# Kernel tuning notes

Measured on AMD Instinct MI355X. Metric: run time of the kernel, lower is better.

The kernel has to match this reference:

```python
import jax, jax.numpy as jnp
import numpy as np

B, N_HEADS, F_TOK = 8, 12, 768
GRID_H, GRID_W = 32, 32
N_TOK = 1 + GRID_H * GRID_W  # 1025 (readout token + patches)
F_HEAD = F_TOK // N_HEADS    # 64
NUM_DIST = (2 * GRID_H - 1) * (2 * GRID_W - 1) + 3  # 3972


def _build_relpos_index(gh, gw):
    # BEiT-style relative position index with 3 extra slots for the readout token
    coords = np.stack(np.meshgrid(np.arange(gh), np.arange(gw), indexing='ij'))  # (2, gh, gw)
    flat = coords.reshape(2, -1)                                                 # (2, gh*gw)
    rel = flat[:, :, None] - flat[:, None, :]                                    # (2, P, P)
    rel = rel.transpose(1, 2, 0).astype(np.int64)                                # (P, P, 2)
    rel[:, :, 0] += gh - 1
    rel[:, :, 1] += gw - 1
    rel[:, :, 0] *= 2 * gw - 1
    rpi = rel.sum(-1)                                                            # (P, P)
    n = 1 + gh * gw
    nd = (2 * gh - 1) * (2 * gw - 1) + 3
    idx = np.zeros((n, n), dtype=np.int32)
    idx[1:, 1:] = rpi
    idx[0, :] = nd - 3  # readout -> all
    idx[:, 0] = nd - 2  # all -> readout
    idx[0, 0] = nd - 1  # readout -> readout
    return idx


def setup_inputs() -> dict:
    key = jax.random.key(0)
    ks = jax.random.split(key, 7)
    tokens = jax.random.normal(ks[0], (B, N_TOK, F_TOK), dtype=jnp.float32)
    qkv_w = jax.random.normal(ks[1], (3 * F_TOK, F_TOK), dtype=jnp.float32) * 0.02
    q_bias = jax.random.normal(ks[2], (1, N_HEADS, 1, F_HEAD), dtype=jnp.float32) * 0.02
    v_bias = jax.random.normal(ks[3], (1, N_HEADS, 1, F_HEAD), dtype=jnp.float32) * 0.02
    relpos_table = jax.random.normal(ks[4], (NUM_DIST, N_HEADS), dtype=jnp.float32) * 0.02
    proj_w = jax.random.normal(ks[5], (F_TOK, F_TOK), dtype=jnp.float32) * 0.02
    proj_b = jax.random.normal(ks[6], (F_TOK,), dtype=jnp.float32) * 0.02
    relpos_index = jnp.asarray(_build_relpos_index(GRID_H, GRID_W))  # (N, N) int32
    return {
        'tokens': tokens, 'qkv_w': qkv_w, 'q_bias': q_bias, 'v_bias': v_bias,
        'relpos_table': relpos_table, 'proj_w': proj_w, 'proj_b': proj_b,
        'relpos_index': relpos_index, 'patch_h': GRID_H, 'patch_w': GRID_W,
    }


def reference(tokens, qkv_w, q_bias, v_bias, relpos_table, proj_w, proj_b,
              relpos_index, patch_h, patch_w):
    b, n, f_tok = tokens.shape
    # qkv projection (no bias): (B, N, 3F) -> (3, B, H, N, f)
    qkv = tokens @ qkv_w.T
    qkv = qkv.reshape(b, n, 3, N_HEADS, F_HEAD).transpose(2, 0, 3, 1, 4)
    q, k, v = qkv[0], qkv[1], qkv[2]
    q = (q + q_bias) * (F_HEAD ** -0.5)
    v = v + v_bias
    # attention scores: (B, H, N, N)
    attn = jnp.einsum('bhnf,bhmf->bhnm', q, k)
    # relative position bias gather: (N, N, H) -> (H, N, N)
    bias = relpos_table[relpos_index].transpose(2, 0, 1)
    attn = attn + bias[None]
    w = jax.nn.softmax(attn, axis=-1)
    out = jnp.einsum('bhnm,bhmf->bhnf', w, v)
    out = out.transpose(0, 2, 1, 3).reshape(b, n, N_HEADS * F_HEAD)
    return out @ proj_w.T + proj_b
```

## Files before the change

### kernel.cpp

```cpp
#include <hip/hip_runtime.h>

#define B_ 8
#define NH 12
#define NTOK 1025
#define FT 768
#define MROWS (B_*NTOK)
#define QPAD 1025
#define CH2 34
#define NQT 36
#define NTT 34
#define NDIST 3972
#define LOG2E 1.44269504089f

typedef __bf16 bf16x8 __attribute__((ext_vector_type(8)));
typedef __bf16 bf16x2 __attribute__((ext_vector_type(2)));
typedef float floatx4 __attribute__((ext_vector_type(4)));
typedef float floatx16 __attribute__((ext_vector_type(16)));
typedef int intx4 __attribute__((ext_vector_type(4)));

__device__ __forceinline__ void async_ld16(const void* gp, void* lp) {
  __builtin_amdgcn_global_load_lds(
      (const __attribute__((address_space(1))) void*)gp,
      (__attribute__((address_space(3))) void*)lp, 16, 0, 0);
}

__global__ __launch_bounds__(256) void cvt_bf16(const float* __restrict__ src,
                                                __bf16* __restrict__ dst, int n4) {
  int i = blockIdx.x * 256 + threadIdx.x;
  if (i >= n4) return;
  float4 v = ((const float4*)src)[i];
  __bf16 o[4] = {(__bf16)v.x, (__bf16)v.y, (__bf16)v.z, (__bf16)v.w};
  *(uint2*)(dst + 4 * (size_t)i) = *(uint2*)o;
}

__global__ __launch_bounds__(256) void table_prep(const float* __restrict__ table,
                                                  __bf16* __restrict__ tableT) {
  int i = blockIdx.x * 256 + threadIdx.x;
  if (i >= NH * NDIST) return;
  int h = i / NDIST, d = i - h * NDIST;
  tableT[i] = (__bf16)(table[(size_t)d * NH + h] * LOG2E);
}

__global__ __launch_bounds__(256) void bias_gather_t(
    const int* __restrict__ idx, const __bf16* __restrict__ tableT,
    __bf16* __restrict__ Bb) {
  __shared__ int ids_l[32][33];
  const int qt = blockIdx.x, tt = blockIdx.y;
  const int t = threadIdx.x;
  {
    const int row = t >> 3, c4 = (t & 7) * 4;
    int qrow = qt * 32 + row; if (qrow > NTOK - 1) qrow = NTOK - 1;
    const int* src = idx + (size_t)qrow * NTOK;
#pragma unroll
    for (int j = 0; j < 4; ++j) {
      int token = tt * 32 + c4 + j; if (token > NTOK - 1) token = NTOK - 1;
      ids_l[row][c4 + j] = src[token];
    }
  }
  __syncthreads();
  const int lane = t & 63, w = t >> 6;
  const int l31 = lane & 31, hb = lane >> 5;
  int ids[16]; bool ok[16];
#pragma unroll
  for (int j = 0; j < 16; ++j) {
    const int col = (j & 3) + 8 * (j >> 2) + 4 * hb;
    ok[j] = tt * 32 + col < NTOK;
    ids[j] = ids_l[l31][col];
  }
#pragma unroll
  for (int g = 0; g < 3; ++g) {
    const int h = w + g * 4;
    const __bf16* tb = tableT + (size_t)h * NDIST;
    __bf16 v[16] __attribute__((aligned(16)));
#pragma unroll
    for (int j = 0; j < 16; ++j)
      v[j] = ok[j] ? tb[ids[j]] : (__bf16)(-1e30f);
    uint4* dst = (uint4*)(Bb + (((size_t)h * NQT + qt) * NTT + tt) * 1024 + lane * 16);
    dst[0] = ((uint4*)v)[0];
    dst[1] = ((uint4*)v)[1];
  }
}

__device__ __forceinline__ void gemm128_pipe(
    const __bf16* __restrict__ A, const __bf16* __restrict__ W,
    int am0, int n0, int amax, __bf16* At, __bf16* Bt, floatx4 acc[4][4]) {
  const int tid = threadIdx.x, wave = tid >> 6, lane = tid & 63;
  const int l = lane & 15, qd = lane >> 4;
  const int wr = wave >> 1, wc = wave & 1;
  const int srow = lane >> 2, sg = lane & 3;
  const int r0 = wave * 32 + srow, r1 = r0 + 16;
  int gm0 = am0 + r0; if (gm0 > amax) gm0 = amax;
  int gm1 = am0 + r1; if (gm1 > amax) gm1 = amax;
  const int sw0 = (sg ^ (r0 & 3)) * 8;
  const __bf16* gA0 = A + (size_t)gm0 * FT + sw0;
  const __bf16* gA1 = A + (size_t)gm1 * FT + sw0;
  const __bf16* gB0 = W + (size_t)(n0 + r0) * FT + sw0;
  const __bf16* gB1 = W + (size_t)(n0 + r1) * FT + sw0;
  const int woff = wave * 32 * 32;
  const int fsw = (qd ^ (l & 3)) * 8;

  auto issue = [&](int k, int buf) {
    __bf16* a = At + buf * 4096 + woff;
    __bf16* b = Bt + buf * 4096 + woff;
    async_ld16(gA0 + k * 32, a);
    async_ld16(gA1 + k * 32, a + 512);
    async_ld16(gB0 + k * 32, b);
    async_ld16(gB1 + k * 32, b + 512);
  };
  auto step = [&](int buf) {
    __builtin_amdgcn_s_barrier();
    const __bf16* ab = At + buf * 4096;
    const __bf16* bb = Bt + buf * 4096;
    bf16x8 aF[4], bF[4];
#pragma unroll
    for (int t = 0; t < 4; ++t)
      aF[t] = *(const bf16x8*)(ab + (wr * 64 + t * 16 + l) * 32 + fsw);
#pragma unroll
    for (int u = 0; u < 4; ++u)
      bF[u] = *(const bf16x8*)(bb + (wc * 64 + u * 16 + l) * 32 + fsw);
#pragma unroll
    for (int t = 0; t < 4; ++t)
#pragma unroll
      for (int u = 0; u < 4; ++u)
        acc[t][u] = __builtin_amdgcn_mfma_f32_16x16x32_bf16(aF[t], bF[u], acc[t][u], 0, 0, 0);
  };

  issue(0, 0);
  issue(1, 1);
  issue(2, 2);
  int b0 = 0, b3 = 3;
  for (int k = 0; k < 24; ++k) {
    if (k < 21) {
      issue(k + 3, b3);
      __builtin_amdgcn_s_waitcnt(0x0F7C);
    } else if (k == 21) {
      __builtin_amdgcn_s_waitcnt(0x0F78);
    } else if (k == 22) {
      __builtin_amdgcn_s_waitcnt(0x0F74);
    } else {
      __builtin_amdgcn_s_waitcnt(0x0F70);
    }
    step(b0);
    ++b0; if (b0 == 5) b0 = 0;
    ++b3; if (b3 == 5) b3 = 0;
  }
}

__global__ __launch_bounds__(256) void qkv_gemm128(
    const __bf16* __restrict__ tokens, const __bf16* __restrict__ qkvw,
    const float* __restrict__ qbias, const float* __restrict__ vbias,
    __bf16* __restrict__ Qb, __bf16* __restrict__ Kc, __bf16* __restrict__ Vc) {
  __shared__ __bf16 At[5 * 4096], Bt[5 * 4096];
  const int u0 = blockIdx.x;
  const int c = u0 & 7, q0 = u0 >> 3;
  const int mt = (q0 / 18) * 8 + c, ni = q0 % 18;
  const int b = mt / 9, ml = mt - b * 9;
  const int am0 = b * NTOK + ml * 128, amax = b * NTOK + 1024;
  const int n0 = ni * 128;
  const int tid = threadIdx.x, wave = tid >> 6, lane = tid & 63;
  const int l = lane & 15, qd = lane >> 4;
  const int wr = wave >> 1, wc = wave & 1;
  floatx4 acc[4][4];
#pragma unroll
  for (int t = 0; t < 4; ++t)
#pragma unroll
    for (int u = 0; u < 4; ++u) acc[t][u] = (floatx4){0.f, 0.f, 0.f, 0.f};
  gemm128_pipe(tokens, qkvw, am0, n0, amax, At, Bt, acc);

  const int which = ni / 6;
  const int nrem0 = (ni - which * 6) * 128;
  const bool full = (ml < 8);
  const int tokb = ml * 128 + wr * 64 + qd * 4;

  if (which == 0) {
#pragma unroll
    for (int u = 0; u < 4; ++u) {
      const int rem = nrem0 + wc * 64 + u * 16 + l;
      const int h = rem >> 6, f = rem & 63;
      const size_t bhq = ((size_t)(b * NH + h)) * QPAD;
      const float qb = qbias[h * 64 + f];
#pragma unroll
      for (int t = 0; t < 4; ++t) {
        const int tok = tokb + t * 16;
        if (full) {
          __bf16* qp = Qb + (bhq + tok) * 64 + f;
#pragma unroll
          for (int r = 0; r < 4; ++r)
            qp[r * 64] = (__bf16)((acc[t][u][r] + qb) * (0.125f * LOG2E));
        } else {
#pragma unroll
          for (int r = 0; r < 4; ++r)
            if (tok + r < NTOK)
              Qb[(bhq + tok + r) * 64 + f] = (__bf16)((acc[t][u][r] + qb) * (0.125f * LOG2E));
        }
      }
    }
  } else if (which == 1) {
#pragma unroll
    for (int u = 0; u < 4; ++u) {
      const int rem = nrem0 + wc * 64 + u * 16 + l;
      const int f = rem & 63;
      const size_t bhc = ((size_t)(b * NH + (rem >> 6))) * CH2;
      const int dgo = (f >> 3) * 256 + (f & 7);
#pragma unroll
      for (int t = 0; t < 4; ++t) {
        const int tok = tokb + t * 16;
        if (full) {
          const size_t base = (bhc + (tok >> 5)) * 2048 + dgo + (tok & 31) * 8;
#pragma unroll
          for (int r = 0; r < 4; ++r) Kc[base + r * 8] = (__bf16)acc[t][u][r];
        } else {
#pragma unroll
          for (int r = 0; r < 4; ++r) {
            const int tk = tok + r;
            if (tk < NTOK)
              Kc[(bhc + (tk >> 5)) * 2048 + (f >> 3) * 256 + (tk & 31) * 8 + (f & 7)] =
                  (__bf16)acc[t][u][r];
          }
        }
      }
    }
  } else {
#pragma unroll
    for (int u = 0; u < 4; ++u) {
      const int rem = nrem0 + wc * 64 + u * 16 + l;
      const int h = rem >> 6, f = rem & 63;
      const size_t bhc = ((size_t)(b * NH + h)) * CH2;
      const float vb = vbias[h * 64 + f];
#pragma unroll
      for (int t = 0; t < 4; ++t) {
        const int tok = tokb + t * 16;
        if (full) {
          __bf16 v4[4] __attribute__((aligned(8)));
#pragma unroll
          for (int r = 0; r < 4; ++r) v4[r] = (__bf16)(acc[t][u][r] + vb);
          const size_t e = (bhc + (tok >> 5)) * 2048 +
                           ((((tok >> 3) & 3) * 64 + f) << 3) + (tok & 7);
          *(uint2*)(Vc + e) = *(const uint2*)v4;
        } else {
#pragma unroll
          for (int r = 0; r < 4; ++r) {
            const int tk = tok + r;
            if (tk < NTOK)
              Vc[(bhc + (tk >> 5)) * 2048 + ((((tk >> 3) & 3) * 64 + f) << 3) + (tk & 7)] =
                  (__bf16)(acc[t][u][r] + vb);
          }
        }
      }
    }
  }
}

__global__ __launch_bounds__(256) void proj_gemm128(
    const __bf16* __restrict__ Ao, const __bf16* __restrict__ projw,
    const float* __restrict__ projb, float* __restrict__ out) {
  __shared__ __bf16 At[5 * 4096], Bt[5 * 4096];
  const int u0 = blockIdx.x;
  const int c = u0 & 7, q0 = u0 >> 3;
  const int mt = (q0 / 6) * 8 + c, ni = q0 % 6;
  const int b = mt / 9, ml = mt - b * 9;
  const int am0 = b * NTOK + ml * 128, amax = b * NTOK + 1024;
  const int n0 = ni * 128;
  const int tid = threadIdx.x, wave = tid >> 6, lane = tid & 63;
  const int l = lane & 15, qd = lane >> 4;
  const int wr = wave >> 1, wc = wave & 1;
  floatx4 acc[4][4];
#pragma unroll
  for (int t = 0; t < 4; ++t)
#pragma unroll
    for (int u = 0; u < 4; ++u) acc[t][u] = (floatx4){0.f, 0.f, 0.f, 0.f};
  gemm128_pipe(Ao, projw, am0, n0, amax, At, Bt, acc);

  const bool full = (ml < 8);
  const int tokb = ml * 128 + wr * 64 + qd * 4;
  const size_t rowb = (size_t)b * NTOK;
#pragma unroll
  for (int u = 0; u < 4; ++u) {
    const int gn = n0 + wc * 64 + u * 16 + l;
    const float pb = projb[gn];
#pragma unroll
    for (int t = 0; t < 4; ++t) {
      const int tok = tokb + t * 16;
      if (full) {
        float* op = out + (rowb + tok) * FT + gn;
#pragma unroll
        for (int r = 0; r < 4; ++r) op[(size_t)r * FT] = acc[t][u][r] + pb;
      } else {
#pragma unroll
        for (int r = 0; r < 4; ++r)
          if (tok + r < NTOK) out[(rowb + tok + r) * FT + gn] = acc[t][u][r] + pb;
      }
    }
  }
}

__global__ __launch_bounds__(256) void attn_flash(
    const __bf16* __restrict__ Qb, const __bf16* __restrict__ Kc,
    const __bf16* __restrict__ Vc, const __bf16* __restrict__ Bb,
    __bf16* __restrict__ Ao) {
  __shared__ __bf16 Kl[5][2048], Vl[5][2048];
  const int bh = blockIdx.x;
  const int h = bh % NH, b = bh / NH;
  const int wave = threadIdx.x >> 6, lane = threadIdx.x & 63;
  const int l31 = lane & 31, hb = lane >> 5;
  const int qt = blockIdx.y * 4 + wave;
  int qrow = qt * 32 + l31; if (qrow > NTOK - 1) qrow = NTOK - 1;

  bf16x8 qf[4];
  {
    const __bf16* Qp = Qb + ((size_t)bh * QPAD + qrow) * 64 + hb * 8;
#pragma unroll
    for (int d = 0; d < 4; ++d) qf[d] = *(const bf16x8*)(Qp + d * 16);
  }

  floatx16 o0, o1;
#pragma unroll
  for (int j = 0; j < 16; ++j) { o0[j] = 0.f; o1[j] = 0.f; }
  float lsum = 0.f;

  const int sw = wave & 1;
  const __bf16* Sg = ((wave < 2) ? Kc : Vc) + (size_t)bh * CH2 * 2048 +
                     sw * 1024 + lane * 8;
  __bf16* Sl0 = ((wave < 2) ? &Kl[0][0] : &Vl[0][0]) + sw * 1024;
  const __bf16* Bg = Bb + ((size_t)h * NQT + qt) * NTT * 1024 + lane * 16;

  auto issueS = [&](int c, int buf) {
    const __bf16* src = Sg + (size_t)c * 2048;
    __bf16* dst = Sl0 + buf * 2048;
    async_ld16(src, dst);
    async_ld16(src + 512, dst + 512);
  };

  auto compute = [&](int buf, bf16x8 cb0, bf16x8 cb1) {
    const __bf16* Kb = &Kl[buf][0];
    const __bf16* Vb = &Vl[buf][0];
    floatx16 st;
#pragma unroll
    for (int j = 0; j < 16; ++j) st[j] = 0.f;
#pragma unroll
    for (int dk = 0; dk < 4; ++dk) {
      bf16x8 a = *(const bf16x8*)(Kb + ((dk * 2 + hb) * 32 + l31) * 8);
      st = __builtin_amdgcn_mfma_f32_32x32x16_bf16(a, qf[dk], st, 0, 0, 0);
    }
    float e[16];
#pragma unroll
    for (int j = 0; j < 16; ++j) {
      const float bj = (float)(j < 8 ? cb0[j] : cb1[j - 8]);
      e[j] = __builtin_amdgcn_exp2f(st[j] + bj);
      lsum += e[j];
    }
    int pk[8];
#pragma unroll
    for (int j2 = 0; j2 < 8; ++j2) {
      bf16x2 pr = {(__bf16)e[2 * j2], (__bf16)e[2 * j2 + 1]};
      pk[j2] = __builtin_bit_cast(int, pr);
    }
#pragma unroll
    for (int ks = 0; ks < 2; ++ks) {
      const int r01a = pk[4 * ks + 0], r01b = pk[4 * ks + 1];
      const int r23a = pk[4 * ks + 2], r23b = pk[4 * ks + 3];
      const int t01a = __shfl_xor(r01a, 32), t01b = __shfl_xor(r01b, 32);
      const int t23a = __shfl_xor(r23a, 32), t23b = __shfl_xor(r23b, 32);
      intx4 fi;
      fi[0] = hb ? t23a : r01a;
      fi[1] = hb ? t23b : r01b;
      fi[2] = hb ? r23a : t01a;
      fi[3] = hb ? r23b : t01b;
      bf16x8 pb = __builtin_bit_cast(bf16x8, fi);
      bf16x8 va0 = *(const bf16x8*)(Vb + ((ks * 2 + hb) * 64 + l31) * 8);
      bf16x8 va1 = *(const bf16x8*)(Vb + ((ks * 2 + hb) * 64 + 32 + l31) * 8);
      o0 = __builtin_amdgcn_mfma_f32_32x32x16_bf16(va0, pb, o0, 0, 0, 0);
      o1 = __builtin_amdgcn_mfma_f32_32x32x16_bf16(va1, pb, o1, 0, 0, 0);
    }
  };

  issueS(0, 0);
  bf16x8 bA0 = *(const bf16x8*)(Bg);
  bf16x8 bA1 = *(const bf16x8*)(Bg + 8);
  issueS(1, 1);
  bf16x8 bB0 = *(const bf16x8*)(Bg + 1024);
  bf16x8 bB1 = *(const bf16x8*)(Bg + 1024 + 8);
  issueS(2, 2);

  int bc = 0;
  for (int ci = 0; ci < 15; ++ci) {
    const int c = 2 * ci;
    __builtin_amdgcn_s_waitcnt(0x0F76);
    __builtin_amdgcn_s_barrier();
    compute(bc, bA0, bA1);
    bA0 = *(const bf16x8*)(Bg + (size_t)(c + 2) * 1024);
    bA1 = *(const bf16x8*)(Bg + (size_t)(c + 2) * 1024 + 8);
    { int b3 = bc + 3; if (b3 >= 5) b3 -= 5; issueS(c + 3, b3); }
    int bc1 = bc + 1; if (bc1 == 5) bc1 = 0;
    __builtin_amdgcn_s_waitcnt(0x0F76);
    __builtin_amdgcn_s_barrier();
    compute(bc1, bB0, bB1);
    bB0 = *(const bf16x8*)(Bg + (size_t)(c + 3) * 1024);
    bB1 = *(const bf16x8*)(Bg + (size_t)(c + 3) * 1024 + 8);
    { int b4 = bc + 4; if (b4 >= 5) b4 -= 5; issueS(c + 4, b4); }
    bc += 2; if (bc >= 5) bc -= 5;
  }
  __builtin_amdgcn_s_waitcnt(0x0F76);
  __builtin_amdgcn_s_barrier();
  compute(0, bA0, bA1);
  bA0 = *(const bf16x8*)(Bg + (size_t)32 * 1024);
  bA1 = *(const bf16x8*)(Bg + (size_t)32 * 1024 + 8);
  issueS(33, 3);
  __builtin_amdgcn_s_waitcnt(0x0F76);
  __builtin_amdgcn_s_barrier();
  compute(1, bB0, bB1);
  bB0 = *(const bf16x8*)(Bg + (size_t)33 * 1024);
  bB1 = *(const bf16x8*)(Bg + (size_t)33 * 1024 + 8);
  __builtin_amdgcn_s_waitcnt(0x0F74);
  __builtin_amdgcn_s_barrier();
  compute(2, bA0, bA1);
  __builtin_amdgcn_s_waitcnt(0x0F70);
  __builtin_amdgcn_s_barrier();
  compute(3, bB0, bB1);

  const float ltot = lsum + __shfl_xor(lsum, 32);
  const float rinv = 1.0f / ltot;
  const int tok = qt * 32 + l31;
  if (tok < NTOK) {
    __bf16* op = Ao + ((size_t)b * NTOK + tok) * FT + h * 64;
#pragma unroll
    for (int ft = 0; ft < 2; ++ft) {
#pragma unroll
      for (int jg = 0; jg < 4; ++jg) {
        const int f = ft * 32 + jg * 8 + hb * 4;
        __bf16 v4[4] __attribute__((aligned(8)));
#pragma unroll
        for (int q = 0; q < 4; ++q) {
          const float ov = ft ? o1[jg * 4 + q] : o0[jg * 4 + q];
          v4[q] = (__bf16)(ov * rinv);
        }
        *(uint2*)(op + f) = *(uint2*)v4;
      }
    }
  }
}

extern "C" void kernel_launch(void* const* d_in, const int* in_sizes, int n_in,
                              void* d_out, int out_size, void* d_ws, size_t ws_size,
                              hipStream_t stream) {
  (void)in_sizes; (void)n_in; (void)out_size; (void)ws_size;
  const float* tokens = (const float*)d_in[0];
  const float* qkvw   = (const float*)d_in[1];
  const float* qbias  = (const float*)d_in[2];
  const float* vbias  = (const float*)d_in[3];
  const float* table  = (const float*)d_in[4];
  const float* projw  = (const float*)d_in[5];
  const float* projb  = (const float*)d_in[6];
  const int*   rpidx  = (const int*)d_in[7];
  float* out = (float*)d_out;
  char* ws = (char*)d_ws;

  const size_t QBQ = (size_t)B_ * NH * QPAD * 64 * 2;
  const size_t KVB = (size_t)B_ * NH * CH2 * 2048 * 2;
  const size_t BBT = (size_t)NH * NQT * NTT * 1024 * 2;
  const size_t AOB = (size_t)MROWS * FT * 2;
  const size_t WQB = (size_t)3 * FT * FT * 2;
  const size_t WPB = (size_t)FT * FT * 2;
  __bf16* Qb = (__bf16*)(ws);
  __bf16* Kc = (__bf16*)(ws + QBQ);
  __bf16* Vc = (__bf16*)(ws + QBQ + KVB);
  __bf16* Bb = (__bf16*)(ws + QBQ + 2 * KVB);
  __bf16* Tb = (__bf16*)(ws + QBQ + 2 * KVB + BBT);
  __bf16* Ao = Tb;
  __bf16* Wq = (__bf16*)(ws + QBQ + 2 * KVB + BBT + AOB);
  __bf16* Wp = (__bf16*)(ws + QBQ + 2 * KVB + BBT + AOB + WQB);
  __bf16* Tt = (__bf16*)(ws + QBQ + 2 * KVB + BBT + AOB + WQB + WPB);

  cvt_bf16<<<(MROWS * FT / 4 + 255) / 256, 256, 0, stream>>>(tokens, Tb, MROWS * FT / 4);
  cvt_bf16<<<(3 * FT * FT / 4 + 255) / 256, 256, 0, stream>>>(qkvw, Wq, 3 * FT * FT / 4);
  cvt_bf16<<<(FT * FT / 4 + 255) / 256, 256, 0, stream>>>(projw, Wp, FT * FT / 4);
  table_prep<<<(NH * NDIST + 255) / 256, 256, 0, stream>>>(table, Tt);
  bias_gather_t<<<dim3(NQT, NTT), 256, 0, stream>>>(rpidx, Tt, Bb);
  qkv_gemm128<<<8 * 9 * 18, 256, 0, stream>>>(Tb, Wq, qbias, vbias, Qb, Kc, Vc);
  attn_flash<<<dim3(B_ * NH, 9), 256, 0, stream>>>(Qb, Kc, Vc, Bb, Ao);
  proj_gemm128<<<8 * 9 * 6, 256, 0, stream>>>(Ao, Wp, projb, out);
}
```

Baseline: 245.7 us.

## Switch projection GEMMs to 256x128 tiles over flattened rows with 512 threads

Both the QKV and output-projection GEMMs move from 128x128 tiles built per batch to 256x128 tiles over the flattened B*N row space, run by 8 waves per block. This removes the per-batch padding waste, since 9 tiles of 128 covered 1025 rows, and loads each weight tile once for twice as many rows. The LDS pipeline shrinks from 5 stages with 3-deep prefetch to 3 stages with 1-deep prefetch, and the XCD-aware block swizzle is dropped. The epilogue becomes generic scalar stores with per-element batch/token decode, giving up the vectorized V store. The __launch_bounds__(512, 4) hint may force heavy register limits and spilling of the 64-float accumulator.

```diff
diff --git a/kernel.cpp b/kernel.cpp
--- a/kernel.cpp
+++ b/kernel.cpp
@@ -81,36 +81,42 @@
   }
 }
 
-__device__ __forceinline__ void gemm128_pipe(
+__device__ __forceinline__ void gemm256_pipe(
     const __bf16* __restrict__ A, const __bf16* __restrict__ W,
-    int am0, int n0, int amax, __bf16* At, __bf16* Bt, floatx4 acc[4][4]) {
+    int am0, int n0, __bf16* Lt, floatx4 acc[4][4]) {
   const int tid = threadIdx.x, wave = tid >> 6, lane = tid & 63;
   const int l = lane & 15, qd = lane >> 4;
+  const int srow = lane >> 2, sg = lane & 3;
+  const int swb = (sg ^ (srow & 3)) * 8;
   const int wr = wave >> 1, wc = wave & 1;
-  const int srow = lane >> 2, sg = lane & 3;
-  const int r0 = wave * 32 + srow, r1 = r0 + 16;
-  int gm0 = am0 + r0; if (gm0 > amax) gm0 = amax;
-  int gm1 = am0 + r1; if (gm1 > amax) gm1 = amax;
-  const int sw0 = (sg ^ (r0 & 3)) * 8;
-  const __bf16* gA0 = A + (size_t)gm0 * FT + sw0;
-  const __bf16* gA1 = A + (size_t)gm1 * FT + sw0;
-  const __bf16* gB0 = W + (size_t)(n0 + r0) * FT + sw0;
-  const __bf16* gB1 = W + (size_t)(n0 + r1) * FT + sw0;
-  const int woff = wave * 32 * 32;
+
+  const __bf16* gsrc[3];
+  int gdst[3];
+#pragma unroll
+  for (int i = 0; i < 3; ++i) {
+    const int g = wave * 3 + i;
+    if (g < 16) {
+      int row = am0 + g * 16 + srow; if (row > MROWS - 1) row = MROWS - 1;
+      gsrc[i] = A + (size_t)row * FT + swb;
+      gdst[i] = g * 512;
+    } else {
+      const int row = n0 + (g - 16) * 16 + srow;
+      gsrc[i] = W + (size_t)row * FT + swb;
+      gdst[i] = 8192 + (g - 16) * 512;
+    }
+  }
   const int fsw = (qd ^ (l & 3)) * 8;
 
   auto issue = [&](int k, int buf) {
-    __bf16* a = At + buf * 4096 + woff;
-    __bf16* b = Bt + buf * 4096 + woff;
-    async_ld16(gA0 + k * 32, a);
-    async_ld16(gA1 + k * 32, a + 512);
-    async_ld16(gB0 + k * 32, b);
-    async_ld16(gB1 + k * 32, b + 512);
+    __bf16* base = Lt + buf * 12288;
+#pragma unroll
+    for (int i = 0; i < 3; ++i)
+      async_ld16(gsrc[i] + k * 32, base + gdst[i]);
   };
   auto step = [&](int buf) {
     __builtin_amdgcn_s_barrier();
-    const __bf16* ab = At + buf * 4096;
-    const __bf16* bb = Bt + buf * 4096;
+    const __bf16* ab = Lt + buf * 12288;
+    const __bf16* bb = ab + 8192;
     bf16x8 aF[4], bF[4];
 #pragma unroll
     for (int t = 0; t < 4; ++t)
@@ -126,37 +132,28 @@
   };
 
   issue(0, 0);
-  issue(1, 1);
-  issue(2, 2);
-  int b0 = 0, b3 = 3;
+  int b0 = 0;
   for (int k = 0; k < 24; ++k) {
-    if (k < 21) {
-      issue(k + 3, b3);
-      __builtin_amdgcn_s_waitcnt(0x0F7C);
-    } else if (k == 21) {
-      __builtin_amdgcn_s_waitcnt(0x0F78);
-    } else if (k == 22) {
-      __builtin_amdgcn_s_waitcnt(0x0F74);
+    if (k < 23) {
+      int b1 = b0 + 1; if (b1 == 3) b1 = 0;
+      issue(k + 1, b1);
+      __builtin_amdgcn_s_waitcnt(0x0F73);
     } else {
       __builtin_amdgcn_s_waitcnt(0x0F70);
     }
     step(b0);
-    ++b0; if (b0 == 5) b0 = 0;
-    ++b3; if (b3 == 5) b3 = 0;
-  }
-}
-
-__global__ __launch_bounds__(256) void qkv_gemm128(
+    ++b0; if (b0 == 3) b0 = 0;
+  }
+}
+
+__global__ __launch_bounds__(512, 4) void qkv_gemm256(
     const __bf16* __restrict__ tokens, const __bf16* __restrict__ qkvw,
     const float* __restrict__ qbias, const float* __restrict__ vbias,
     __bf16* __restrict__ Qb, __bf16* __restrict__ Kc, __bf16* __restrict__ Vc) {
-  __shared__ __bf16 At[5 * 4096], Bt[5 * 4096];
+  __shared__ __bf16 Lt[3 * 12288];
   const int u0 = blockIdx.x;
-  const int c = u0 & 7, q0 = u0 >> 3;
-  const int mt = (q0 / 18) * 8 + c, ni = q0 % 18;
-  const int b = mt / 9, ml = mt - b * 9;
-  const int am0 = b * NTOK + ml * 128, amax = b * NTOK + 1024;
-  const int n0 = ni * 128;
+  const int mt = u0 / 18, ni = u0 % 18;
+  const int am0 = mt * 256, n0 = ni * 128;
   const int tid = threadIdx.x, wave = tid >> 6, lane = tid & 63;
   const int l = lane & 15, qd = lane >> 4;
   const int wr = wave >> 1, wc = wave & 1;
@@ -165,102 +162,50 @@
   for (int t = 0; t < 4; ++t)
 #pragma unroll
     for (int u = 0; u < 4; ++u) acc[t][u] = (floatx4){0.f, 0.f, 0.f, 0.f};
-  gemm128_pipe(tokens, qkvw, am0, n0, amax, At, Bt, acc);
+  gemm256_pipe(tokens, qkvw, am0, n0, Lt, acc);
 
   const int which = ni / 6;
   const int nrem0 = (ni - which * 6) * 128;
-  const bool full = (ml < 8);
-  const int tokb = ml * 128 + wr * 64 + qd * 4;
-
-  if (which == 0) {
-#pragma unroll
-    for (int u = 0; u < 4; ++u) {
-      const int rem = nrem0 + wc * 64 + u * 16 + l;
-      const int h = rem >> 6, f = rem & 63;
-      const size_t bhq = ((size_t)(b * NH + h)) * QPAD;
-      const float qb = qbias[h * 64 + f];
-#pragma unroll
-      for (int t = 0; t < 4; ++t) {
-        const int tok = tokb + t * 16;
-        if (full) {
-          __bf16* qp = Qb + (bhq + tok) * 64 + f;
-#pragma unroll
-          for (int r = 0; r < 4; ++r)
-            qp[r * 64] = (__bf16)((acc[t][u][r] + qb) * (0.125f * LOG2E));
+#pragma unroll
+  for (int u = 0; u < 4; ++u) {
+    const int rem = nrem0 + wc * 64 + u * 16 + l;
+    const int h = rem >> 6, f = rem & 63;
+    const float qb = (which == 0) ? qbias[h * 64 + f] : 0.f;
+    const float vb = (which == 2) ? vbias[h * 64 + f] : 0.f;
+#pragma unroll
+    for (int t = 0; t < 4; ++t) {
+      const int gmb = am0 + wr * 64 + t * 16 + qd * 4;
+#pragma unroll
+      for (int r = 0; r < 4; ++r) {
+        const int gm = gmb + r;
+        if (gm >= MROWS) continue;
+        const int b = (int)(((unsigned)gm * 16369u) >> 24);
+        const int tok = gm - b * 1025;
+        const size_t bh = (size_t)(b * NH + h);
+        const float v = acc[t][u][r];
+        if (which == 0) {
+          Qb[(bh * QPAD + tok) * 64 + f] = (__bf16)((v + qb) * (0.125f * LOG2E));
+        } else if (which == 1) {
+          const size_t e = (bh * CH2 + (tok >> 5)) * 2048 +
+                           (f >> 3) * 256 + (tok & 31) * 8 + (f & 7);
+          Kc[e] = (__bf16)v;
         } else {
-#pragma unroll
-          for (int r = 0; r < 4; ++r)
-            if (tok + r < NTOK)
-              Qb[(bhq + tok + r) * 64 + f] = (__bf16)((acc[t][u][r] + qb) * (0.125f * LOG2E));
+          const size_t e = (bh * CH2 + (tok >> 5)) * 2048 +
+                           (((tok >> 3) & 3) * 64 + f) * 8 + (tok & 7);
+          Vc[e] = (__bf16)(v + vb);
         }
       }
     }
-  } else if (which == 1) {
-#pragma unroll
-    for (int u = 0; u < 4; ++u) {
-      const int rem = nrem0 + wc * 64 + u * 16 + l;
-      const int f = rem & 63;
-      const size_t bhc = ((size_t)(b * NH + (rem >> 6))) * CH2;
-      const int dgo = (f >> 3) * 256 + (f & 7);
-#pragma unroll
-      for (int t = 0; t < 4; ++t) {
-        const int tok = tokb + t * 16;
-        if (full) {
-          const size_t base = (bhc + (tok >> 5)) * 2048 + dgo + (tok & 31) * 8;
-#pragma unroll
-          for (int r = 0; r < 4; ++r) Kc[base + r * 8] = (__bf16)acc[t][u][r];
-        } else {
-#pragma unroll
-          for (int r = 0; r < 4; ++r) {
-            const int tk = tok + r;
-            if (tk < NTOK)
-              Kc[(bhc + (tk >> 5)) * 2048 + (f >> 3) * 256 + (tk & 31) * 8 + (f & 7)] =
-                  (__bf16)acc[t][u][r];
-          }
-        }
-      }
-    }
-  } else {
-#pragma unroll
-    for (int u = 0; u < 4; ++u) {
-      const int rem = nrem0 + wc * 64 + u * 16 + l;
-      const int h = rem >> 6, f = rem & 63;
-      const size_t bhc = ((size_t)(b * NH + h)) * CH2;
-      const float vb = vbias[h * 64 + f];
-#pragma unroll
-      for (int t = 0; t < 4; ++t) {
-        const int tok = tokb + t * 16;
-        if (full) {
-          __bf16 v4[4] __attribute__((aligned(8)));
-#pragma unroll
-          for (int r = 0; r < 4; ++r) v4[r] = (__bf16)(acc[t][u][r] + vb);
-          const size_t e = (bhc + (tok >> 5)) * 2048 +
-                           ((((tok >> 3) & 3) * 64 + f) << 3) + (tok & 7);
-          *(uint2*)(Vc + e) = *(const uint2*)v4;
-        } else {
-#pragma unroll
-          for (int r = 0; r < 4; ++r) {
-            const int tk = tok + r;
-            if (tk < NTOK)
-              Vc[(bhc + (tk >> 5)) * 2048 + ((((tk >> 3) & 3) * 64 + f) << 3) + (tk & 7)] =
-                  (__bf16)(acc[t][u][r] + vb);
-          }
-        }
-      }
-    }
-  }
-}
-
-__global__ __launch_bounds__(256) void proj_gemm128(
+  }
+}
+
+__global__ __launch_bounds__(512, 4) void proj_gemm256(
     const __bf16* __restrict__ Ao, const __bf16* __restrict__ projw,
     const float* __restrict__ projb, float* __restrict__ out) {
-  __shared__ __bf16 At[5 * 4096], Bt[5 * 4096];
+  __shared__ __bf16 Lt[3 * 12288];
   const int u0 = blockIdx.x;
-  const int c = u0 & 7, q0 = u0 >> 3;
-  const int mt = (q0 / 6) * 8 + c, ni = q0 % 6;
-  const int b = mt / 9, ml = mt - b * 9;
-  const int am0 = b * NTOK + ml * 128, amax = b * NTOK + 1024;
-  const int n0 = ni * 128;
+  const int mt = u0 / 6, ni = u0 % 6;
+  const int am0 = mt * 256, n0 = ni * 128;
   const int tid = threadIdx.x, wave = tid >> 6, lane = tid & 63;
   const int l = lane & 15, qd = lane >> 4;
   const int wr = wave >> 1, wc = wave & 1;
@@ -269,26 +214,19 @@
   for (int t = 0; t < 4; ++t)
 #pragma unroll
     for (int u = 0; u < 4; ++u) acc[t][u] = (floatx4){0.f, 0.f, 0.f, 0.f};
-  gemm128_pipe(Ao, projw, am0, n0, amax, At, Bt, acc);
-
-  const bool full = (ml < 8);
-  const int tokb = ml * 128 + wr * 64 + qd * 4;
-  const size_t rowb = (size_t)b * NTOK;
+  gemm256_pipe(Ao, projw, am0, n0, Lt, acc);
+
 #pragma unroll
   for (int u = 0; u < 4; ++u) {
     const int gn = n0 + wc * 64 + u * 16 + l;
     const float pb = projb[gn];
 #pragma unroll
     for (int t = 0; t < 4; ++t) {
-      const int tok = tokb + t * 16;
-      if (full) {
-        float* op = out + (rowb + tok) * FT + gn;
-#pragma unroll
-        for (int r = 0; r < 4; ++r) op[(size_t)r * FT] = acc[t][u][r] + pb;
-      } else {
-#pragma unroll
-        for (int r = 0; r < 4; ++r)
-          if (tok + r < NTOK) out[(rowb + tok + r) * FT + gn] = acc[t][u][r] + pb;
+      const int gmb = am0 + wr * 64 + t * 16 + qd * 4;
+#pragma unroll
+      for (int r = 0; r < 4; ++r) {
+        const int gm = gmb + r;
+        if (gm < MROWS) out[(size_t)gm * FT + gn] = acc[t][u][r] + pb;
       }
     }
   }
@@ -476,7 +414,7 @@
   cvt_bf16<<<(FT * FT / 4 + 255) / 256, 256, 0, stream>>>(projw, Wp, FT * FT / 4);
   table_prep<<<(NH * NDIST + 255) / 256, 256, 0, stream>>>(table, Tt);
   bias_gather_t<<<dim3(NQT, NTT), 256, 0, stream>>>(rpidx, Tt, Bb);
-  qkv_gemm128<<<8 * 9 * 18, 256, 0, stream>>>(Tb, Wq, qbias, vbias, Qb, Kc, Vc);
+  qkv_gemm256<<<33 * 18, 512, 0, stream>>>(Tb, Wq, qbias, vbias, Qb, Kc, Vc);
   attn_flash<<<dim3(B_ * NH, 9), 256, 0, stream>>>(Qb, Kc, Vc, Bb, Ao);
-  proj_gemm128<<<8 * 9 * 6, 256, 0, stream>>>(Ao, Wp, projb, out);
-}
+  proj_gemm256<<<33 * 6, 512, 0, stream>>>(Ao, Wp, projb, out);
+}
```

After: 253.9 us. 3.4% more time.
